# Performance work log

Measured on AMD Instinct MI355X. Metric: run time of the kernel, lower is better.

The kernel has to match this reference:

```python
import jax, jax.numpy as jnp
import numpy as np

T, B, D = 2048, 8, 1024
INIT_ALPHA_BIAS = 2.0


def setup_inputs() -> dict:
    key = jax.random.key(0)
    k1, k2, k3, k4 = jax.random.split(key, 4)
    xav = float(np.sqrt(6.0 / (D + D)))  # xavier_uniform bound
    return {
        "x": jax.random.normal(k1, (T, B, D), dtype=jnp.float32),
        "h0": jax.random.normal(k2, (B, D), dtype=jnp.float32),
        "W_alpha": jax.random.uniform(k3, (D, D), jnp.float32, -xav, xav),
        "b_alpha": jnp.full((D,), INIT_ALPHA_BIAS, dtype=jnp.float32),
        "W_v": jax.random.uniform(k4, (D, D), jnp.float32, -xav, xav),
        "b_v": jnp.zeros((D,), dtype=jnp.float32),
    }


def reference(x, h0, W_alpha, b_alpha, W_v, b_v):
    # Gates/values for all timesteps at once (batched GEMMs): [T, B, D]
    alpha = jax.nn.sigmoid(jnp.einsum("tbd,ed->tbe", x, W_alpha) + b_alpha)
    v = jnp.einsum("tbd,ed->tbe", x, W_v) + b_v

    def step(h_prev, av):
        a_t, v_t = av
        h_new = a_t * h_prev + (1.0 - a_t) * v_t
        out_t = h_new * jax.nn.silu(h_new)
        return h_new, (h_new, out_t)

    _, (hs, output) = jax.lax.scan(step, h0, (alpha, v))
    h = jnp.concatenate([h0[None], hs], axis=0)  # [T+1, B, D]
    return output, h
```

## Files before the change

### kernel.cpp

```cpp
#include <hip/hip_runtime.h>
#include <hip/hip_bf16.h>

#define T_DIM 2048
#define B_DIM 8
#define D_DIM 1024
#define M_DIM (T_DIM * B_DIM)
#define K_DIM D_DIM
#define NW_DIM (2 * D_DIM)
#define NCH (B_DIM * D_DIM)
#define NCH4 (NCH / 4)
#define CHUNKS 64
#define CHUNK_LEN 32

typedef __attribute__((ext_vector_type(8))) short bf16x8;
typedef __attribute__((ext_vector_type(4))) float f32x4;

__device__ __forceinline__ unsigned short bf16_rne(float f) {
    unsigned u = __float_as_uint(f);
    unsigned r = u + 0x7fffu + ((u >> 16) & 1u);
    return (unsigned short)(r >> 16);
}

__device__ __forceinline__ float sigmoidf(float z) {
    return 1.0f / (1.0f + __expf(-z));
}

__device__ __forceinline__ void load_lds16(const void* g, void* l) {
    __builtin_amdgcn_global_load_lds(
        (const __attribute__((address_space(1))) void*)g,
        (__attribute__((address_space(3))) void*)l,
        16, 0, 0);
}

__global__ __launch_bounds__(256) void convert_all_kernel(
    const float4* __restrict__ x,
    const float4* __restrict__ Wa,
    const float4* __restrict__ Wv,
    ushort4* __restrict__ xb,
    ushort4* __restrict__ Wcat) {
    const int nx4 = M_DIM * K_DIM / 4;
    const int half4 = D_DIM * D_DIM / 4;
    int i = blockIdx.x * 256 + threadIdx.x;
    float4 f;
    ushort4* __restrict__ dst;
    int di;
    if (i < nx4) {
        f = x[i];
        dst = xb;
        di = i;
    } else {
        int j = i - nx4;
        f = (j < half4) ? Wa[j] : Wv[j - half4];
        dst = Wcat;
        di = j;
    }
    ushort4 o;
    o.x = bf16_rne(f.x);
    o.y = bf16_rne(f.y);
    o.z = bf16_rne(f.z);
    o.w = bf16_rne(f.w);
    dst[di] = o;
}

#define MMA_QUAD(IB)                                                        \
    _Pragma("unroll") for (int i = 0; i < 4; ++i)                           \
    _Pragma("unroll") for (int j = 0; j < 4; ++j)                           \
        acc[(IB) + i][j] = __builtin_amdgcn_mfma_f32_16x16x32_bf16(         \
            af[i], bf[j], acc[(IB) + i][j], 0, 0, 0);

__global__ __launch_bounds__(512, 2) void gemm_fused_kernel(
    const unsigned short* __restrict__ A,
    const unsigned short* __restrict__ W,
    const float* __restrict__ ba,
    const float* __restrict__ bv,
    float* __restrict__ alpha_dst,
    float* __restrict__ v_dst) {
    extern __shared__ __attribute__((aligned(16))) char smem[];

    const int tid = threadIdx.x;
    const int lane = tid & 63;
    const int w = tid >> 6;
    const int wm = w >> 2;
    const int wn = w & 3;
    const int quad = lane >> 4;
    const int l16 = lane & 15;

    const int bid = blockIdx.x;
    const int swz = (bid & 7) * 64 + (bid >> 3);
    const int bx = swz & 7;
    const int by = swz >> 3;
    const int bm = by * 256;
    const int bn = bx * 256;

    const int vsw = (((l16 & 1) << 2) | quad) ^ (l16 >> 1);
    const int rdA = wm * 8192 + (l16 >> 1) * 128 + vsw * 16;
    const int rdB = wn * 4096 + (l16 >> 1) * 128 + vsw * 16;

    const int p = lane & 7;
    const int hl = lane >> 3;
    const int vp = p ^ hl;
    const int qsrc = vp & 3;
    const int rb = (vp >> 2) & 1;
    const int r0 = 16 * (2 * w + 0) + 2 * hl + rb;
    const int r1 = 16 * (2 * w + 1) + 2 * hl + rb;
    const char* Ab = (const char*)A;
    const char* Wb = (const char*)W;
    const size_t offA0 = (size_t)(bm + r0) * 2048 + (size_t)qsrc * 16;
    const size_t offA1 = (size_t)(bm + r1) * 2048 + (size_t)qsrc * 16;
    const size_t offB0 = (size_t)(bn + r0) * 2048 + (size_t)qsrc * 16;
    const size_t offB1 = (size_t)(bn + r1) * 2048 + (size_t)qsrc * 16;
    const int lds0 = (2 * w + 0) * 1024;
    const int lds1 = (2 * w + 1) * 1024;

    f32x4 acc[8][4];
    bf16x8 af[4], bf[4];
    {
        f32x4 zero = {0.f, 0.f, 0.f, 0.f};
#pragma unroll
        for (int i = 0; i < 8; ++i)
#pragma unroll
            for (int j = 0; j < 4; ++j) acc[i][j] = zero;
    }

    auto stage_a = [&](int buf, int ts) {
        char* base = smem + (buf << 15);
        load_lds16(Ab + offA0 + (size_t)ts * 64, base + lds0);
        load_lds16(Ab + offA1 + (size_t)ts * 64, base + lds1);
    };
    auto stage_b = [&](int buf, int ts) {
        char* base = smem + (buf << 15) + 16384;
        load_lds16(Wb + offB0 + (size_t)ts * 64, base + lds0);
        load_lds16(Wb + offB1 + (size_t)ts * 64, base + lds1);
    };
    auto read_a = [&](int buf, int ib) {
        const char* la = smem + (buf << 15);
#pragma unroll
        for (int i = 0; i < 4; ++i)
            af[i] = *(const bf16x8*)(la + rdA + (ib + i) * 1024);
    };
    auto read_b = [&](int buf) {
        const char* lb = smem + (buf << 15) + 16384;
#pragma unroll
        for (int j = 0; j < 4; ++j)
            bf[j] = *(const bf16x8*)(lb + rdB + j * 1024);
    };

    auto phaseA = [&](int t, bool do_stage) {
        const int buf = t & 3;
        read_a(buf, 0);
        read_b(buf);
        if (do_stage) stage_a((t + 3) & 3, t + 3);
        asm volatile("s_waitcnt lgkmcnt(0)" ::: "memory");
        __builtin_amdgcn_sched_barrier(0);
        __builtin_amdgcn_s_setprio(1);
        MMA_QUAD(0)
        __builtin_amdgcn_s_setprio(0);
        __builtin_amdgcn_s_barrier();
    };
    auto phaseB = [&](int t, bool do_stage, int vm) {
        const int buf = t & 3;
        read_a(buf, 4);
        if (do_stage) stage_b((t + 3) & 3, t + 3);
        if (vm == 8) asm volatile("s_waitcnt vmcnt(8)" ::: "memory");
        else if (vm == 4) asm volatile("s_waitcnt vmcnt(4)" ::: "memory");
        else if (vm == 0) asm volatile("s_waitcnt vmcnt(0)" ::: "memory");
        asm volatile("s_waitcnt lgkmcnt(0)" ::: "memory");
        __builtin_amdgcn_sched_barrier(0);
        __builtin_amdgcn_s_setprio(1);
        MMA_QUAD(4)
        __builtin_amdgcn_s_setprio(0);
        __builtin_amdgcn_s_barrier();
    };

    stage_a(0, 0); stage_b(0, 0);
    stage_a(1, 1); stage_b(1, 1);
    stage_a(2, 2); stage_b(2, 2);
    asm volatile("s_waitcnt vmcnt(8)" ::: "memory");
    __builtin_amdgcn_s_barrier();

    for (int t = 0; t < 29; ++t) {
        phaseA(t, true);
        phaseB(t, true, 8);
    }
    phaseA(29, false);
    phaseB(29, false, 4);
    phaseA(30, false);
    phaseB(30, false, 0);
    phaseA(31, false);
    phaseB(31, false, -1);

    const bool is_alpha = (bn < D_DIM);
    float* __restrict__ dst = is_alpha ? alpha_dst : v_dst;
    const float* __restrict__ bias = is_alpha ? ba : bv;
    const int nb = bn - (is_alpha ? 0 : D_DIM);
#pragma unroll
    for (int j = 0; j < 4; ++j) {
        const int n = nb + wn * 64 + j * 16 + l16;
        const float bias_n = bias[n];
#pragma unroll
        for (int i = 0; i < 8; ++i) {
            const int m0 = bm + wm * 128 + i * 16 + quad * 4;
#pragma unroll
            for (int r = 0; r < 4; ++r) {
                float val = acc[i][j][r] + bias_n;
                if (is_alpha) val = sigmoidf(val);
                dst[(size_t)(m0 + r) * D_DIM + n] = val;
            }
        }
    }
}


__global__ __launch_bounds__(256) void scan_phase1_kernel(
    const float4* __restrict__ alpha,
    const float4* __restrict__ v,
    float4* __restrict__ P,
    float4* __restrict__ Q) {
    const int j4 = blockIdx.x * 256 + threadIdx.x;
    const int c = blockIdx.y;
    float4 Pr = {1.f, 1.f, 1.f, 1.f};
    float4 Qr = {0.f, 0.f, 0.f, 0.f};
    size_t base = (size_t)c * CHUNK_LEN * NCH4 + j4;
#pragma unroll 4
    for (int t = 0; t < CHUNK_LEN; ++t) {
        float4 a = alpha[base + (size_t)t * NCH4];
        float4 vv = v[base + (size_t)t * NCH4];
        Pr.x *= a.x; Pr.y *= a.y; Pr.z *= a.z; Pr.w *= a.w;
        Qr.x = a.x * Qr.x + (1.f - a.x) * vv.x;
        Qr.y = a.y * Qr.y + (1.f - a.y) * vv.y;
        Qr.z = a.z * Qr.z + (1.f - a.z) * vv.z;
        Qr.w = a.w * Qr.w + (1.f - a.w) * vv.w;
    }
    P[(size_t)c * NCH4 + j4] = Pr;
    Q[(size_t)c * NCH4 + j4] = Qr;
}

__global__ __launch_bounds__(256) void scan_phase2_kernel(
    const float* __restrict__ P, const float* __restrict__ Q,
    const float* __restrict__ h0,
    float* __restrict__ Hc,
    float* __restrict__ hbase) {
    const int ch = blockIdx.x * 256 + threadIdx.x;
    float h = h0[ch];
    hbase[ch] = h;
#pragma unroll 8
    for (int c = 0; c < CHUNKS; ++c) {
        Hc[(size_t)c * NCH + ch] = h;
        h = P[(size_t)c * NCH + ch] * h + Q[(size_t)c * NCH + ch];
    }
}

__global__ __launch_bounds__(256) void scan_phase3_kernel(
    float4* __restrict__ alpha_out,
    float4* __restrict__ v_h,
    const float4* __restrict__ Hc) {
    const int j4 = blockIdx.x * 256 + threadIdx.x;
    const int c = blockIdx.y;
    float4 h = Hc[(size_t)c * NCH4 + j4];
    size_t base = (size_t)c * CHUNK_LEN * NCH4 + j4;
#pragma unroll 4
    for (int t = 0; t < CHUNK_LEN; ++t) {
        float4 a = alpha_out[base + (size_t)t * NCH4];
        float4 vv = v_h[base + (size_t)t * NCH4];
        h.x = a.x * h.x + (1.f - a.x) * vv.x;
        h.y = a.y * h.y + (1.f - a.y) * vv.y;
        h.z = a.z * h.z + (1.f - a.z) * vv.z;
        h.w = a.w * h.w + (1.f - a.w) * vv.w;
        float4 o;
        o.x = h.x * h.x * sigmoidf(h.x);
        o.y = h.y * h.y * sigmoidf(h.y);
        o.z = h.z * h.z * sigmoidf(h.z);
        o.w = h.w * h.w * sigmoidf(h.w);
        alpha_out[base + (size_t)t * NCH4] = o;
        v_h[base + (size_t)t * NCH4] = h;
    }
}

extern "C" void kernel_launch(void* const* d_in, const int* in_sizes, int n_in,
                              void* d_out, int out_size, void* d_ws, size_t ws_size,
                              hipStream_t stream) {
    const float* x  = (const float*)d_in[0];
    const float* h0 = (const float*)d_in[1];
    const float* Wa = (const float*)d_in[2];
    const float* ba = (const float*)d_in[3];
    const float* Wv = (const float*)d_in[4];
    const float* bv = (const float*)d_in[5];

    float* out = (float*)d_out;
    float* hbase = out + (size_t)T_DIM * NCH;
    float* alpha = out;
    float* vbuf = hbase + NCH;

    char* ws = (char*)d_ws;
    unsigned short* xb   = (unsigned short*)ws;
    unsigned short* Wcat = (unsigned short*)(ws + 33554432);
    float* P  = (float*)(ws + 37748736);
    float* Q  = (float*)(ws + 39845888);
    float* Hc = (float*)(ws + 41943040);

    static bool attr_done = false;
    if (!attr_done) {
        hipFuncSetAttribute(reinterpret_cast<const void*>(gemm_fused_kernel),
                            hipFuncAttributeMaxDynamicSharedMemorySize, 131072);
        attr_done = true;
    }

    const int nconv = (M_DIM * K_DIM / 4) + (2 * D_DIM * D_DIM / 4);
    convert_all_kernel<<<nconv / 256, 256, 0, stream>>>(
        (const float4*)x, (const float4*)Wa, (const float4*)Wv,
        (ushort4*)xb, (ushort4*)Wcat);

    gemm_fused_kernel<<<512, 512, 131072, stream>>>(xb, Wcat, ba, bv, alpha, vbuf);

    dim3 sgrid(NCH4 / 256, CHUNKS);
    scan_phase1_kernel<<<sgrid, 256, 0, stream>>>(
        (const float4*)alpha, (const float4*)vbuf, (float4*)P, (float4*)Q);
    scan_phase2_kernel<<<NCH / 256, 256, 0, stream>>>(
        P, Q, h0, Hc, hbase);
    scan_phase3_kernel<<<sgrid, 256, 0, stream>>>(
        (float4*)alpha, (float4*)vbuf, (const float4*)Hc);
}
```

Before: 320.8 us.

## Shrink GEMM tile to 128x256 with 3-stage pipeline for higher occupancy

Halves the M tile of the fused projection GEMM from 256 to 128 rows, doubling the grid to 1024 blocks and raising launch bounds to 4 waves per SIMD. The LDS pipeline drops from 4 buffers to 3, with one combined stage per K step, and the wait and barrier placement moves to after the MFMA block. The aim is more resident blocks and fewer accumulator registers to hide memory latency better. The cost is lower reuse of each B tile and more global loads per FLOP.

```diff
diff --git a/kernel.cpp b/kernel.cpp
--- a/kernel.cpp
+++ b/kernel.cpp
@@ -62,13 +62,7 @@
     dst[di] = o;
 }
 
-#define MMA_QUAD(IB)                                                        \
-    _Pragma("unroll") for (int i = 0; i < 4; ++i)                           \
-    _Pragma("unroll") for (int j = 0; j < 4; ++j)                           \
-        acc[(IB) + i][j] = __builtin_amdgcn_mfma_f32_16x16x32_bf16(         \
-            af[i], bf[j], acc[(IB) + i][j], 0, 0, 0);
-
-__global__ __launch_bounds__(512, 2) void gemm_fused_kernel(
+__global__ __launch_bounds__(512, 4) void gemm_fused_kernel(
     const unsigned short* __restrict__ A,
     const unsigned short* __restrict__ W,
     const float* __restrict__ ba,
@@ -86,108 +80,90 @@
     const int l16 = lane & 15;
 
     const int bid = blockIdx.x;
-    const int swz = (bid & 7) * 64 + (bid >> 3);
+    const int swz = (bid & 7) * 128 + (bid >> 3);
     const int bx = swz & 7;
     const int by = swz >> 3;
-    const int bm = by * 256;
+    const int bm = by * 128;
     const int bn = bx * 256;
 
     const int vsw = (((l16 & 1) << 2) | quad) ^ (l16 >> 1);
-    const int rdA = wm * 8192 + (l16 >> 1) * 128 + vsw * 16;
+    const int rdA = wm * 4096 + (l16 >> 1) * 128 + vsw * 16;
     const int rdB = wn * 4096 + (l16 >> 1) * 128 + vsw * 16;
 
-    const int p = lane & 7;
     const int hl = lane >> 3;
-    const int vp = p ^ hl;
+    const int vp = (lane & 7) ^ hl;
     const int qsrc = vp & 3;
     const int rb = (vp >> 2) & 1;
-    const int r0 = 16 * (2 * w + 0) + 2 * hl + rb;
-    const int r1 = 16 * (2 * w + 1) + 2 * hl + rb;
+    const int rA  = 16 * w + 2 * hl + rb;
+    const int rB0 = 32 * w + 2 * hl + rb;
+    const int rB1 = rB0 + 16;
     const char* Ab = (const char*)A;
     const char* Wb = (const char*)W;
-    const size_t offA0 = (size_t)(bm + r0) * 2048 + (size_t)qsrc * 16;
-    const size_t offA1 = (size_t)(bm + r1) * 2048 + (size_t)qsrc * 16;
-    const size_t offB0 = (size_t)(bn + r0) * 2048 + (size_t)qsrc * 16;
-    const size_t offB1 = (size_t)(bn + r1) * 2048 + (size_t)qsrc * 16;
-    const int lds0 = (2 * w + 0) * 1024;
-    const int lds1 = (2 * w + 1) * 1024;
-
-    f32x4 acc[8][4];
-    bf16x8 af[4], bf[4];
+    const size_t offA  = (size_t)(bm + rA ) * 2048 + (size_t)qsrc * 16;
+    const size_t offB0 = (size_t)(bn + rB0) * 2048 + (size_t)qsrc * 16;
+    const size_t offB1 = (size_t)(bn + rB1) * 2048 + (size_t)qsrc * 16;
+    const int ldsA  = w * 1024;
+    const int ldsB0 = (2 * w) * 1024;
+    const int ldsB1 = (2 * w + 1) * 1024;
+
+    f32x4 acc[4][4];
     {
         f32x4 zero = {0.f, 0.f, 0.f, 0.f};
 #pragma unroll
-        for (int i = 0; i < 8; ++i)
+        for (int i = 0; i < 4; ++i)
 #pragma unroll
             for (int j = 0; j < 4; ++j) acc[i][j] = zero;
     }
 
-    auto stage_a = [&](int buf, int ts) {
-        char* base = smem + (buf << 15);
-        load_lds16(Ab + offA0 + (size_t)ts * 64, base + lds0);
-        load_lds16(Ab + offA1 + (size_t)ts * 64, base + lds1);
+    auto stage = [&](int buf, int t) {
+        char* bA = smem + buf * 24576;
+        char* bB = bA + 8192;
+        const size_t ko = (size_t)t * 64;
+        load_lds16(Ab + offA + ko, bA + ldsA);
+        load_lds16(Wb + offB0 + ko, bB + ldsB0);
+        load_lds16(Wb + offB1 + ko, bB + ldsB1);
     };
-    auto stage_b = [&](int buf, int ts) {
-        char* base = smem + (buf << 15) + 16384;
-        load_lds16(Wb + offB0 + (size_t)ts * 64, base + lds0);
-        load_lds16(Wb + offB1 + (size_t)ts * 64, base + lds1);
-    };
-    auto read_a = [&](int buf, int ib) {
-        const char* la = smem + (buf << 15);
+
+    auto tile_step = [&](int buf, int nbuf, int tn, bool do_stage, int vm,
+                         bool bar) {
+        const char* bA = smem + buf * 24576;
+        const char* bB = bA + 8192;
+        bf16x8 af[4], bfr[4];
 #pragma unroll
         for (int i = 0; i < 4; ++i)
-            af[i] = *(const bf16x8*)(la + rdA + (ib + i) * 1024);
-    };
-    auto read_b = [&](int buf) {
-        const char* lb = smem + (buf << 15) + 16384;
+            af[i] = *(const bf16x8*)(bA + rdA + i * 1024);
 #pragma unroll
         for (int j = 0; j < 4; ++j)
-            bf[j] = *(const bf16x8*)(lb + rdB + j * 1024);
-    };
-
-    auto phaseA = [&](int t, bool do_stage) {
-        const int buf = t & 3;
-        read_a(buf, 0);
-        read_b(buf);
-        if (do_stage) stage_a((t + 3) & 3, t + 3);
+            bfr[j] = *(const bf16x8*)(bB + rdB + j * 1024);
+        if (do_stage) stage(nbuf, tn);
         asm volatile("s_waitcnt lgkmcnt(0)" ::: "memory");
         __builtin_amdgcn_sched_barrier(0);
         __builtin_amdgcn_s_setprio(1);
-        MMA_QUAD(0)
+#pragma unroll
+        for (int i = 0; i < 4; ++i)
+#pragma unroll
+            for (int j = 0; j < 4; ++j)
+                acc[i][j] = __builtin_amdgcn_mfma_f32_16x16x32_bf16(
+                    af[i], bfr[j], acc[i][j], 0, 0, 0);
         __builtin_amdgcn_s_setprio(0);
-        __builtin_amdgcn_s_barrier();
+        if (vm == 3) asm volatile("s_waitcnt vmcnt(3)" ::: "memory");
+        else if (vm == 0) asm volatile("s_waitcnt vmcnt(0)" ::: "memory");
+        if (bar) __builtin_amdgcn_s_barrier();
     };
-    auto phaseB = [&](int t, bool do_stage, int vm) {
-        const int buf = t & 3;
-        read_a(buf, 4);
-        if (do_stage) stage_b((t + 3) & 3, t + 3);
-        if (vm == 8) asm volatile("s_waitcnt vmcnt(8)" ::: "memory");
-        else if (vm == 4) asm volatile("s_waitcnt vmcnt(4)" ::: "memory");
-        else if (vm == 0) asm volatile("s_waitcnt vmcnt(0)" ::: "memory");
-        asm volatile("s_waitcnt lgkmcnt(0)" ::: "memory");
-        __builtin_amdgcn_sched_barrier(0);
-        __builtin_amdgcn_s_setprio(1);
-        MMA_QUAD(4)
-        __builtin_amdgcn_s_setprio(0);
-        __builtin_amdgcn_s_barrier();
-    };
-
-    stage_a(0, 0); stage_b(0, 0);
-    stage_a(1, 1); stage_b(1, 1);
-    stage_a(2, 2); stage_b(2, 2);
-    asm volatile("s_waitcnt vmcnt(8)" ::: "memory");
+
+    stage(0, 0);
+    stage(1, 1);
+    asm volatile("s_waitcnt vmcnt(3)" ::: "memory");
     __builtin_amdgcn_s_barrier();
 
-    for (int t = 0; t < 29; ++t) {
-        phaseA(t, true);
-        phaseB(t, true, 8);
-    }
-    phaseA(29, false);
-    phaseB(29, false, 4);
-    phaseA(30, false);
-    phaseB(30, false, 0);
-    phaseA(31, false);
-    phaseB(31, false, -1);
+    for (int it = 0; it < 10; ++it) {
+        const int t = it * 3;
+        tile_step(0, 2, t + 2, true, 3, true);
+        tile_step(1, 0, t + 3, true, 3, true);
+        tile_step(2, 1, t + 4, true, 3, true);
+    }
+    tile_step(0, 0, 0, false, 0, true);
+    tile_step(1, 0, 0, false, -1, false);
 
     const bool is_alpha = (bn < D_DIM);
     float* __restrict__ dst = is_alpha ? alpha_dst : v_dst;
@@ -198,8 +174,8 @@
         const int n = nb + wn * 64 + j * 16 + l16;
         const float bias_n = bias[n];
 #pragma unroll
-        for (int i = 0; i < 8; ++i) {
-            const int m0 = bm + wm * 128 + i * 16 + quad * 4;
+        for (int i = 0; i < 4; ++i) {
+            const int m0 = bm + wm * 64 + i * 16 + quad * 4;
 #pragma unroll
             for (int r = 0; r < 4; ++r) {
                 float val = acc[i][j][r] + bias_n;
@@ -301,7 +277,7 @@
     static bool attr_done = false;
     if (!attr_done) {
         hipFuncSetAttribute(reinterpret_cast<const void*>(gemm_fused_kernel),
-                            hipFuncAttributeMaxDynamicSharedMemorySize, 131072);
+                            hipFuncAttributeMaxDynamicSharedMemorySize, 73728);
         attr_done = true;
     }
 
@@ -310,7 +286,8 @@
         (const float4*)x, (const float4*)Wa, (const float4*)Wv,
         (ushort4*)xb, (ushort4*)Wcat);
 
-    gemm_fused_kernel<<<512, 512, 131072, stream>>>(xb, Wcat, ba, bv, alpha, vbuf);
+    gemm_fused_kernel<<<1024, 512, 73728, stream>>>(xb, Wcat, ba, bv, alpha,
+                                                    vbuf);
 
     dim3 sgrid(NCH4 / 256, CHUNKS);
     scan_phase1_kernel<<<sgrid, 256, 0, stream>>>(
```

Measured after the change: 315.8 us. About the same (-1.6%).
